# Optimization experiments

Hardware: AMD Instinct MI355X
Metric: run time of the kernel (lower is better)

The kernel has to match this reference:

```python
import jax, jax.numpy as jnp
import numpy as np

B, N, D = 256, 512, 64  # batch, positions, channels; units = spatial_units = D


def setup_inputs() -> dict:
    key = jax.random.key(0)
    ks = jax.random.split(key, 9)
    g = 1.0 / np.sqrt(D)  # glorot-ish scale for square matrices
    return {
        "x": jax.random.normal(ks[0], (B, N, D), dtype=jnp.float32),
        "Wq_t": jax.random.normal(ks[1], (D, D), dtype=jnp.float32) * g,
        "Wk_t": jax.random.normal(ks[2], (D, D), dtype=jnp.float32) * g,
        "Wv_t": jax.random.normal(ks[3], (D, D), dtype=jnp.float32) * g,
        "Wq_s": jax.random.normal(ks[4], (D, D), dtype=jnp.float32) * g,
        "Wk_s": jax.random.normal(ks[5], (D, D), dtype=jnp.float32) * g,
        "Wv_s": jax.random.normal(ks[6], (D, D), dtype=jnp.float32) * g,
        "Wd_t": jax.random.normal(ks[7], (D, D), dtype=jnp.float32) * g,
        "bd_t": jnp.zeros((D,), dtype=jnp.float32),
        "Wd_s": jax.random.normal(ks[8], (D, D), dtype=jnp.float32) * g,
        "bd_s": jnp.zeros((D,), dtype=jnp.float32),
    }


def _branch(x, Wq, Wk, Wv, Wd, bd):
    # x: [B, N, D]; one self-attention branch followed by a Dense layer.
    q = jnp.einsum("bnd,de->bne", x, Wq)
    k = jnp.einsum("bnd,de->bne", x, Wk)
    v = jnp.einsum("bnd,de->bne", x, Wv)
    scale = 1.0 / jnp.sqrt(jnp.asarray(Wk.shape[-1], dtype=x.dtype))
    scores = jnp.einsum("bne,bme->bnm", q, k) * scale  # [B, N, N]
    w = jax.nn.softmax(scores, axis=-1)
    attn = jnp.einsum("bnm,bmd->bnd", w, v)
    return jnp.einsum("bnd,de->bne", attn, Wd) + bd


def reference(x, Wq_t, Wk_t, Wv_t, Wq_s, Wk_s, Wv_s, Wd_t, bd_t, Wd_s, bd_s):
    temporal = _branch(x, Wq_t, Wk_t, Wv_t, Wd_t, bd_t)
    spatial = _branch(x, Wq_s, Wk_s, Wv_s, Wd_s, bd_s)
    gate = jax.nn.sigmoid(temporal + spatial)
    return x * gate
```

## Files before the change

### kernel.cpp

```cpp
#include <hip/hip_runtime.h>

typedef __attribute__((ext_vector_type(8))) short short8;
typedef __attribute__((ext_vector_type(4))) short short4v;
typedef __attribute__((ext_vector_type(4))) float float4v;

#define MFMA16(a, b, c) __builtin_amdgcn_mfma_f32_16x16x32_bf16((a), (b), (c), 0, 0, 0)

constexpr int kThreads = 512;
constexpr int LDS_TOTAL_BYTES = 163840;

static __device__ __forceinline__ unsigned short f2bf(float f) {
  unsigned int u = __float_as_uint(f);
  u = (u + 0x7fffu + ((u >> 16) & 1u)) >> 16;
  return (unsigned short)u;
}

static __device__ __forceinline__ int wsw_idx(int e, int d) {
  return ((((d >> 3) << 9) + (e << 3) + (d & 7)) ^ (((d >> 3) & 3) << 3));
}

__global__ __launch_bounds__(kThreads, 2) void ts_attn_fused(
    const float* __restrict__ x, const float* __restrict__ Wq_t,
    const float* __restrict__ Wk_t, const float* __restrict__ Wv_t,
    const float* __restrict__ Wq_s, const float* __restrict__ Wk_s,
    const float* __restrict__ Wv_s, const float* __restrict__ Wd_t,
    const float* __restrict__ bd_t, const float* __restrict__ Wd_s,
    const float* __restrict__ bd_s, float* __restrict__ out,
    unsigned short* __restrict__ qws) {
  extern __shared__ __align__(16) unsigned short smem[];
  unsigned short* Ksw = smem;
  unsigned short* Vsw = smem + 32768;
  unsigned short* Wst = smem + 65536;
  unsigned short* Wdsw = smem + 77824;

  const int tid = threadIdx.x;
  const int wv = tid >> 6;
  const int lane = tid & 63;
  const int ln = lane & 15;
  const int quad = lane >> 4;
  const int e8 = ln & 7;
  const int b = blockIdx.x;

  const float* xb = x + (size_t)b * (512 * 64);
  float* outb = out + (size_t)b * (512 * 64);
  unsigned short* qg = qws + (size_t)b * (512 * 64);

#pragma unroll 1
  for (int br = 0; br < 2; ++br) {
    const float* Wq = br ? Wq_s : Wq_t;
    const float* Wk = br ? Wk_s : Wk_t;
    const float* Wv = br ? Wv_s : Wv_t;
    const float* Wd = br ? Wd_s : Wd_t;

    {
      const int d = tid >> 3;
      const int e0 = (tid & 7) * 8;
      const float* srcs[3] = {Wq, Wk, Wv};
#pragma unroll
      for (int g = 0; g < 3; ++g) {
        const float4v u = *reinterpret_cast<const float4v*>(srcs[g] + d * 64 + e0);
        const float4v v = *reinterpret_cast<const float4v*>(srcs[g] + d * 64 + e0 + 4);
        unsigned short* dst = Wst + g * 4096;
#pragma unroll
        for (int i = 0; i < 4; ++i) dst[wsw_idx(e0 + i, d)] = f2bf(u[i]);
#pragma unroll
        for (int i = 0; i < 4; ++i) dst[wsw_idx(e0 + 4 + i, d)] = f2bf(v[i]);
      }
      const int cp_ = d >> 5;
      const int c = d & 31;
      const int qd_ = (c >> 2) & 3;
      const int h_ = ((c >> 4) << 2) | (c & 3);
      const int gbase = (cp_ * 4 + qd_);
      const float4v u = *reinterpret_cast<const float4v*>(Wd + d * 64 + e0);
      const float4v v = *reinterpret_cast<const float4v*>(Wd + d * 64 + e0 + 4);
#pragma unroll
      for (int i = 0; i < 4; ++i) {
        const int e = e0 + i;
        Wdsw[e * 64 + ((gbase ^ (e & 7)) << 3) + h_] = f2bf(u[i]);
      }
#pragma unroll
      for (int i = 0; i < 4; ++i) {
        const int e = e0 + 4 + i;
        Wdsw[e * 64 + ((gbase ^ (e & 7)) << 3) + h_] = f2bf(v[i]);
      }
    }
    __syncthreads();

#pragma unroll 1
    for (int mi = 0; mi < 4; ++mi) {
      const int mrow = (wv + mi * 8) * 16 + ln;
      const int kpq = mrow >> 5;
      const int w5 = mrow & 31;
      const int jj = ((w5 >> 4) << 2) | (w5 & 3);
      const int qg2 = (w5 >> 2) & 3;
      short8 xa0, xa1;
      {
        const float4v u0 = *reinterpret_cast<const float4v*>(xb + mrow * 64 + quad * 8);
        const float4v v0 = *reinterpret_cast<const float4v*>(xb + mrow * 64 + quad * 8 + 4);
        const float4v u1 = *reinterpret_cast<const float4v*>(xb + mrow * 64 + 32 + quad * 8);
        const float4v v1 = *reinterpret_cast<const float4v*>(xb + mrow * 64 + 32 + quad * 8 + 4);
#pragma unroll
        for (int i = 0; i < 4; ++i) {
          xa0[i] = (short)f2bf(u0[i]);
          xa0[4 + i] = (short)f2bf(v0[i]);
          xa1[i] = (short)f2bf(u1[i]);
          xa1[4 + i] = (short)f2bf(v1[i]);
        }
      }
#pragma unroll
      for (int g = 0; g < 3; ++g) {
        const unsigned short* Wg = Wst + g * 4096;
#pragma unroll
        for (int nt = 0; nt < 4; ++nt) {
          const short8 w0 = *reinterpret_cast<const short8*>(Wg + wsw_idx(nt * 16 + ln, quad * 8));
          const short8 w1 = *reinterpret_cast<const short8*>(Wg + wsw_idx(nt * 16 + ln, 32 + quad * 8));
          float4v acc = {0.f, 0.f, 0.f, 0.f};
          acc = MFMA16(w0, xa0, acc);
          acc = MFMA16(w1, xa1, acc);
          if (g == 0) {
            short4v pk;
#pragma unroll
            for (int r = 0; r < 4; ++r) pk[r] = (short)f2bf(acc[r]);
            *reinterpret_cast<short4v*>(
                qg + mrow * 64 + (nt >> 1) * 32 + quad * 8 + (nt & 1) * 4) = pk;
          } else if (g == 1) {
            short4v pk;
#pragma unroll
            for (int r = 0; r < 4; ++r) pk[r] = (short)f2bf(acc[r]);
            const int gswz = ((nt >> 1) * 4 + quad) ^ (mrow & 7);
            *reinterpret_cast<short4v*>(
                Ksw + mrow * 64 + (gswz << 3) + (nt & 1) * 4) = pk;
          } else {
#pragma unroll
            for (int r = 0; r < 4; ++r) {
              const int d = nt * 16 + quad * 4 + r;
              const int gv = (kpq ^ (d & 7) ^ qg2);
              Vsw[(d << 9) + (qg2 << 7) + (gv << 3) + jj] = f2bf(acc[r]);
            }
          }
        }
      }
    }
    __syncthreads();

#pragma unroll 1
    for (int qi = 0; qi < 2; ++qi) {
      const int qtA = wv + qi * 16;
      const int qtB = wv + 8 + qi * 16;
      const unsigned short* qrowA = qg + (qtA * 16 + ln) * 64;
      const unsigned short* qrowB = qg + (qtB * 16 + ln) * 64;
      const short8 qaA = *reinterpret_cast<const short8*>(qrowA + quad * 8);
      const short8 qbA = *reinterpret_cast<const short8*>(qrowA + 32 + quad * 8);
      const short8 qaB = *reinterpret_cast<const short8*>(qrowB + quad * 8);
      const short8 qbB = *reinterpret_cast<const short8*>(qrowB + 32 + quad * 8);

      const int kb0 = ln * 64 + ((quad ^ e8) << 3);
      const int kb1 = ln * 64 + (((4 + quad) ^ e8) << 3);
      const int vxor = (quad << 3) ^ (e8 << 3);

      float4v oA[4], oB[4];
#pragma unroll
      for (int i = 0; i < 4; ++i) {
        oA[i] = (float4v){0.f, 0.f, 0.f, 0.f};
        oB[i] = (float4v){0.f, 0.f, 0.f, 0.f};
      }
      float mrunA = -3.0e38f, mrunB = -3.0e38f;
      float sumA = 0.f, sumB = 0.f;

#pragma unroll 1
      for (int ch = 0; ch < 8; ++ch) {
        float4v sA[4], sB[4];
#pragma unroll
        for (int k8 = 0; k8 < 4; ++k8) {
          const int kt = ch * 4 + k8;
          const short8 k0 = *reinterpret_cast<const short8*>(Ksw + kt * 1024 + kb0);
          const short8 k1 = *reinterpret_cast<const short8*>(Ksw + kt * 1024 + kb1);
          float4v aA = {0.f, 0.f, 0.f, 0.f};
          aA = MFMA16(k0, qaA, aA);
          aA = MFMA16(k1, qbA, aA);
          sA[k8] = aA;
          float4v aB = {0.f, 0.f, 0.f, 0.f};
          aB = MFMA16(k0, qaB, aB);
          aB = MFMA16(k1, qbB, aB);
          sB[k8] = aB;
        }

        float4v m4A = sA[0], m4B = sB[0];
#pragma unroll
        for (int k8 = 1; k8 < 4; ++k8)
#pragma unroll
          for (int r = 0; r < 4; ++r) {
            m4A[r] = fmaxf(m4A[r], sA[k8][r]);
            m4B[r] = fmaxf(m4B[r], sB[k8][r]);
          }
        float cmxA = fmaxf(fmaxf(m4A[0], m4A[1]), fmaxf(m4A[2], m4A[3]));
        float cmxB = fmaxf(fmaxf(m4B[0], m4B[1]), fmaxf(m4B[2], m4B[3]));
        cmxA = fmaxf(cmxA, __shfl_xor(cmxA, 16, 64));
        cmxB = fmaxf(cmxB, __shfl_xor(cmxB, 16, 64));
        cmxA = fmaxf(cmxA, __shfl_xor(cmxA, 32, 64));
        cmxB = fmaxf(cmxB, __shfl_xor(cmxB, 32, 64));

        const float mnewA = fmaxf(mrunA, cmxA);
        const float mnewB = fmaxf(mrunB, cmxB);
        const float scaleA = __expf((mrunA - mnewA) * 0.125f);
        const float scaleB = __expf((mrunB - mnewB) * 0.125f);
        sumA *= scaleA;
        sumB *= scaleB;
#pragma unroll
        for (int i = 0; i < 4; ++i)
#pragma unroll
          for (int r = 0; r < 4; ++r) {
            oA[i][r] *= scaleA;
            oB[i][r] *= scaleB;
          }
        const float offsA = -mnewA * 0.125f;
        const float offsB = -mnewB * 0.125f;
        mrunA = mnewA;
        mrunB = mnewB;

#pragma unroll
        for (int kp = 0; kp < 2; ++kp) {
          float pA[8], pB[8];
#pragma unroll
          for (int h = 0; h < 2; ++h) {
            const int k8 = kp * 2 + h;
#pragma unroll
            for (int r = 0; r < 4; ++r) {
              pA[h * 4 + r] = __expf(fmaf(sA[k8][r], 0.125f, offsA));
              pB[h * 4 + r] = __expf(fmaf(sB[k8][r], 0.125f, offsB));
            }
          }
          sumA += ((pA[0] + pA[4]) + (pA[1] + pA[5])) + ((pA[2] + pA[6]) + (pA[3] + pA[7]));
          sumB += ((pB[0] + pB[4]) + (pB[1] + pB[5])) + ((pB[2] + pB[6]) + (pB[3] + pB[7]));
          short8 pfA, pfB;
#pragma unroll
          for (int j = 0; j < 8; ++j) {
            pfA[j] = (short)f2bf(pA[j]);
            pfB[j] = (short)f2bf(pB[j]);
          }
          const int kpg = ch * 2 + kp;
#pragma unroll
          for (int nto = 0; nto < 4; ++nto) {
            const int vb = (nto * 16 + ln) * 512 + quad * 128;
            const short8 vf = *reinterpret_cast<const short8*>(
                Vsw + vb + (((kpg << 3) ^ vxor)));
            oA[nto] = MFMA16(vf, pfA, oA[nto]);
            oB[nto] = MFMA16(vf, pfB, oB[nto]);
          }
        }
      }

      sumA += __shfl_xor(sumA, 16, 64);
      sumB += __shfl_xor(sumB, 16, 64);
      sumA += __shfl_xor(sumA, 32, 64);
      sumB += __shfl_xor(sumB, 32, 64);
      const float invA = 1.0f / sumA;
      const float invB = 1.0f / sumB;

      short8 of0A, of1A, of0B, of1B;
#pragma unroll
      for (int r = 0; r < 4; ++r) {
        of0A[r] = (short)f2bf(oA[0][r] * invA);
        of0A[4 + r] = (short)f2bf(oA[1][r] * invA);
        of1A[r] = (short)f2bf(oA[2][r] * invA);
        of1A[4 + r] = (short)f2bf(oA[3][r] * invA);
        of0B[r] = (short)f2bf(oB[0][r] * invB);
        of0B[4 + r] = (short)f2bf(oB[1][r] * invB);
        of1B[r] = (short)f2bf(oB[2][r] * invB);
        of1B[4 + r] = (short)f2bf(oB[3][r] * invB);
      }

#pragma unroll
      for (int nt = 0; nt < 4; ++nt) {
        const int ebase = (nt * 16 + ln) * 64;
        const short8 w0 = *reinterpret_cast<const short8*>(
            Wdsw + ebase + ((quad ^ e8) << 3));
        const short8 w1 = *reinterpret_cast<const short8*>(
            Wdsw + ebase + (((4 + quad) ^ e8) << 3));
        float4v accA = {0.f, 0.f, 0.f, 0.f};
        accA = MFMA16(w0, of0A, accA);
        accA = MFMA16(w1, of1A, accA);
        float4v accB = {0.f, 0.f, 0.f, 0.f};
        accB = MFMA16(w0, of0B, accB);
        accB = MFMA16(w1, of1B, accB);
        const int e0 = nt * 16 + quad * 4;
#pragma unroll
        for (int t = 0; t < 2; ++t) {
          const int row = (t == 0 ? qtA : qtB) * 16 + ln;
          const float4v acc = t == 0 ? accA : accB;
          float4v* op = reinterpret_cast<float4v*>(outb + row * 64 + e0);
          if (br == 0) {
            *op = acc;
          } else {
            const float4v bt = *reinterpret_cast<const float4v*>(bd_t + e0);
            const float4v bs = *reinterpret_cast<const float4v*>(bd_s + e0);
            const float4v parked = *op;
            const float4v xv = *reinterpret_cast<const float4v*>(xb + row * 64 + e0);
            float4v res;
#pragma unroll
            for (int r = 0; r < 4; ++r) {
              const float z = parked[r] + acc[r] + bt[r] + bs[r];
              const float gate = 1.0f / (1.0f + __expf(-z));
              res[r] = xv[r] * gate;
            }
            *op = res;
          }
        }
      }
    }
    __syncthreads();
  }
}

extern "C" void kernel_launch(void* const* d_in, const int* in_sizes, int n_in,
                              void* d_out, int out_size, void* d_ws, size_t ws_size,
                              hipStream_t stream) {
  const float* x = (const float*)d_in[0];
  const float* Wq_t = (const float*)d_in[1];
  const float* Wk_t = (const float*)d_in[2];
  const float* Wv_t = (const float*)d_in[3];
  const float* Wq_s = (const float*)d_in[4];
  const float* Wk_s = (const float*)d_in[5];
  const float* Wv_s = (const float*)d_in[6];
  const float* Wd_t = (const float*)d_in[7];
  const float* bd_t = (const float*)d_in[8];
  const float* Wd_s = (const float*)d_in[9];
  const float* bd_s = (const float*)d_in[10];
  float* out = (float*)d_out;
  unsigned short* qws = (unsigned short*)d_ws;

  hipFuncSetAttribute(reinterpret_cast<const void*>(ts_attn_fused),
                      hipFuncAttributeMaxDynamicSharedMemorySize, LDS_TOTAL_BYTES);
  ts_attn_fused<<<dim3(256), dim3(kThreads), LDS_TOTAL_BYTES, stream>>>(
      x, Wq_t, Wk_t, Wv_t, Wq_s, Wk_s, Wv_s, Wd_t, bd_t, Wd_s, bd_s, out, qws);
}
```

Measured before the change: 184.7 us.

## Split each batch across two blocks with half-size K/V LDS streaming

Launches two blocks per batch element, each owning half of the query rows, and halves the LDS footprint by holding only 256 keys of K/V at a time. The block processes the key range in two passes, recomputing K/V for the second half and restaging weights into two small slots in between. This doubles the grid and allows more resident blocks per CU, at the cost of duplicated K/V projection work and extra barriers. It also swaps the manual float-to-bf16 rounding for the native __bf16 conversion.

Measured after the change: 209.8 us. +13.6%, slower.

```diff
diff --git a/kernel.cpp b/kernel.cpp
--- a/kernel.cpp
+++ b/kernel.cpp
@@ -7,12 +7,11 @@
 #define MFMA16(a, b, c) __builtin_amdgcn_mfma_f32_16x16x32_bf16((a), (b), (c), 0, 0, 0)
 
 constexpr int kThreads = 512;
-constexpr int LDS_TOTAL_BYTES = 163840;
+constexpr int LDS_TOTAL_BYTES = 81920;
 
 static __device__ __forceinline__ unsigned short f2bf(float f) {
-  unsigned int u = __float_as_uint(f);
-  u = (u + 0x7fffu + ((u >> 16) & 1u)) >> 16;
-  return (unsigned short)u;
+  __bf16 h = (__bf16)f;
+  return __builtin_bit_cast(unsigned short, h);
 }
 
 static __device__ __forceinline__ int wsw_idx(int e, int d) {
@@ -29,9 +28,9 @@
     unsigned short* __restrict__ qws) {
   extern __shared__ __align__(16) unsigned short smem[];
   unsigned short* Ksw = smem;
-  unsigned short* Vsw = smem + 32768;
-  unsigned short* Wst = smem + 65536;
-  unsigned short* Wdsw = smem + 77824;
+  unsigned short* Vsw = smem + 16384;
+  unsigned short* slotA = smem + 32768;
+  unsigned short* slotB = smem + 36864;
 
   const int tid = threadIdx.x;
   const int wv = tid >> 6;
@@ -39,11 +38,96 @@
   const int ln = lane & 15;
   const int quad = lane >> 4;
   const int e8 = ln & 7;
-  const int b = blockIdx.x;
+  const int bp = blockIdx.x;
+  const int b = bp >> 1;
+  const int h = bp & 1;
 
   const float* xb = x + (size_t)b * (512 * 64);
   float* outb = out + (size_t)b * (512 * 64);
   unsigned short* qg = qws + (size_t)b * (512 * 64);
+
+  const int kb0 = ln * 64 + ((quad ^ e8) << 3);
+  const int kb1 = ln * 64 + (((4 + quad) ^ e8) << 3);
+  const int vxor = (quad << 3) ^ (e8 << 3);
+
+  auto stageW = [&](const float* W, unsigned short* dst) {
+    const int d = tid >> 3;
+    const int e0 = (tid & 7) * 8;
+    const float4v u = *reinterpret_cast<const float4v*>(W + d * 64 + e0);
+    const float4v v = *reinterpret_cast<const float4v*>(W + d * 64 + e0 + 4);
+#pragma unroll
+    for (int i = 0; i < 4; ++i) dst[wsw_idx(e0 + i, d)] = f2bf(u[i]);
+#pragma unroll
+    for (int i = 0; i < 4; ++i) dst[wsw_idx(e0 + 4 + i, d)] = f2bf(v[i]);
+  };
+  auto stageWd = [&](const float* W, unsigned short* dst) {
+    const int d = tid >> 3;
+    const int e0 = (tid & 7) * 8;
+    const int cp_ = d >> 5;
+    const int c = d & 31;
+    const int qd_ = (c >> 2) & 3;
+    const int h_ = ((c >> 4) << 2) | (c & 3);
+    const int gbase = cp_ * 4 + qd_;
+    const float4v u = *reinterpret_cast<const float4v*>(W + d * 64 + e0);
+    const float4v v = *reinterpret_cast<const float4v*>(W + d * 64 + e0 + 4);
+#pragma unroll
+    for (int i = 0; i < 4; ++i) {
+      const int e = e0 + i;
+      dst[e * 64 + ((gbase ^ (e & 7)) << 3) + h_] = f2bf(u[i]);
+    }
+#pragma unroll
+    for (int i = 0; i < 4; ++i) {
+      const int e = e0 + 4 + i;
+      dst[e * 64 + ((gbase ^ (e & 7)) << 3) + h_] = f2bf(v[i]);
+    }
+  };
+  auto loadX = [&](int grow, short8& xa0, short8& xa1) {
+    const float4v u0 = *reinterpret_cast<const float4v*>(xb + grow * 64 + quad * 8);
+    const float4v v0 = *reinterpret_cast<const float4v*>(xb + grow * 64 + quad * 8 + 4);
+    const float4v u1 = *reinterpret_cast<const float4v*>(xb + grow * 64 + 32 + quad * 8);
+    const float4v v1 = *reinterpret_cast<const float4v*>(xb + grow * 64 + 32 + quad * 8 + 4);
+#pragma unroll
+    for (int i = 0; i < 4; ++i) {
+      xa0[i] = (short)f2bf(u0[i]);
+      xa0[4 + i] = (short)f2bf(v0[i]);
+      xa1[i] = (short)f2bf(u1[i]);
+      xa1[4 + i] = (short)f2bf(v1[i]);
+    }
+  };
+  auto mmW = [&](const unsigned short* Wl, const short8& xa0, const short8& xa1,
+                 int nt) -> float4v {
+    const short8 w0 = *reinterpret_cast<const short8*>(Wl + wsw_idx(nt * 16 + ln, quad * 8));
+    const short8 w1 = *reinterpret_cast<const short8*>(Wl + wsw_idx(nt * 16 + ln, 32 + quad * 8));
+    float4v acc = {0.f, 0.f, 0.f, 0.f};
+    acc = MFMA16(w0, xa0, acc);
+    acc = MFMA16(w1, xa1, acc);
+    return acc;
+  };
+  auto writeQ = [&](int grow, int nt, float4v acc) {
+    short4v pk;
+#pragma unroll
+    for (int r = 0; r < 4; ++r) pk[r] = (short)f2bf(acc[r]);
+    *reinterpret_cast<short4v*>(qg + grow * 64 + (nt >> 1) * 32 + quad * 8 + (nt & 1) * 4) = pk;
+  };
+  auto writeK = [&](int lrow, int nt, float4v acc) {
+    short4v pk;
+#pragma unroll
+    for (int r = 0; r < 4; ++r) pk[r] = (short)f2bf(acc[r]);
+    const int gswz = ((nt >> 1) * 4 + quad) ^ (lrow & 7);
+    *reinterpret_cast<short4v*>(Ksw + lrow * 64 + (gswz << 3) + (nt & 1) * 4) = pk;
+  };
+  auto writeV = [&](int lrow, int nt, float4v acc) {
+    const int kpqL = lrow >> 5;
+    const int w5 = lrow & 31;
+    const int jj = ((w5 >> 4) << 2) | (w5 & 3);
+    const int qg2 = (w5 >> 2) & 3;
+#pragma unroll
+    for (int r = 0; r < 4; ++r) {
+      const int d = nt * 16 + quad * 4 + r;
+      const int gv = kpqL ^ (d & 7) ^ qg2;
+      Vsw[(d << 8) + (qg2 << 6) + (gv << 3) + jj] = f2bf(acc[r]);
+    }
+  };
 
 #pragma unroll 1
   for (int br = 0; br < 2; ++br) {
@@ -52,123 +136,62 @@
     const float* Wv = br ? Wv_s : Wv_t;
     const float* Wd = br ? Wd_s : Wd_t;
 
-    {
-      const int d = tid >> 3;
-      const int e0 = (tid & 7) * 8;
-      const float* srcs[3] = {Wq, Wk, Wv};
-#pragma unroll
-      for (int g = 0; g < 3; ++g) {
-        const float4v u = *reinterpret_cast<const float4v*>(srcs[g] + d * 64 + e0);
-        const float4v v = *reinterpret_cast<const float4v*>(srcs[g] + d * 64 + e0 + 4);
-        unsigned short* dst = Wst + g * 4096;
-#pragma unroll
-        for (int i = 0; i < 4; ++i) dst[wsw_idx(e0 + i, d)] = f2bf(u[i]);
-#pragma unroll
-        for (int i = 0; i < 4; ++i) dst[wsw_idx(e0 + 4 + i, d)] = f2bf(v[i]);
-      }
-      const int cp_ = d >> 5;
-      const int c = d & 31;
-      const int qd_ = (c >> 2) & 3;
-      const int h_ = ((c >> 4) << 2) | (c & 3);
-      const int gbase = (cp_ * 4 + qd_);
-      const float4v u = *reinterpret_cast<const float4v*>(Wd + d * 64 + e0);
-      const float4v v = *reinterpret_cast<const float4v*>(Wd + d * 64 + e0 + 4);
-#pragma unroll
-      for (int i = 0; i < 4; ++i) {
-        const int e = e0 + i;
-        Wdsw[e * 64 + ((gbase ^ (e & 7)) << 3) + h_] = f2bf(u[i]);
-      }
-#pragma unroll
-      for (int i = 0; i < 4; ++i) {
-        const int e = e0 + 4 + i;
-        Wdsw[e * 64 + ((gbase ^ (e & 7)) << 3) + h_] = f2bf(v[i]);
-      }
-    }
-    __syncthreads();
-
-#pragma unroll 1
-    for (int mi = 0; mi < 4; ++mi) {
-      const int mrow = (wv + mi * 8) * 16 + ln;
-      const int kpq = mrow >> 5;
-      const int w5 = mrow & 31;
-      const int jj = ((w5 >> 4) << 2) | (w5 & 3);
-      const int qg2 = (w5 >> 2) & 3;
+    stageW(Wq, slotA);
+    stageW(Wk, slotB);
+    __syncthreads();
+
+#pragma unroll 1
+    for (int i = 0; i < 2; ++i) {
+      const int grow = (h * 16 + wv + i * 8) * 16 + ln;
       short8 xa0, xa1;
-      {
-        const float4v u0 = *reinterpret_cast<const float4v*>(xb + mrow * 64 + quad * 8);
-        const float4v v0 = *reinterpret_cast<const float4v*>(xb + mrow * 64 + quad * 8 + 4);
-        const float4v u1 = *reinterpret_cast<const float4v*>(xb + mrow * 64 + 32 + quad * 8);
-        const float4v v1 = *reinterpret_cast<const float4v*>(xb + mrow * 64 + 32 + quad * 8 + 4);
-#pragma unroll
-        for (int i = 0; i < 4; ++i) {
-          xa0[i] = (short)f2bf(u0[i]);
-          xa0[4 + i] = (short)f2bf(v0[i]);
-          xa1[i] = (short)f2bf(u1[i]);
-          xa1[4 + i] = (short)f2bf(v1[i]);
-        }
-      }
-#pragma unroll
-      for (int g = 0; g < 3; ++g) {
-        const unsigned short* Wg = Wst + g * 4096;
-#pragma unroll
-        for (int nt = 0; nt < 4; ++nt) {
-          const short8 w0 = *reinterpret_cast<const short8*>(Wg + wsw_idx(nt * 16 + ln, quad * 8));
-          const short8 w1 = *reinterpret_cast<const short8*>(Wg + wsw_idx(nt * 16 + ln, 32 + quad * 8));
-          float4v acc = {0.f, 0.f, 0.f, 0.f};
-          acc = MFMA16(w0, xa0, acc);
-          acc = MFMA16(w1, xa1, acc);
-          if (g == 0) {
-            short4v pk;
-#pragma unroll
-            for (int r = 0; r < 4; ++r) pk[r] = (short)f2bf(acc[r]);
-            *reinterpret_cast<short4v*>(
-                qg + mrow * 64 + (nt >> 1) * 32 + quad * 8 + (nt & 1) * 4) = pk;
-          } else if (g == 1) {
-            short4v pk;
-#pragma unroll
-            for (int r = 0; r < 4; ++r) pk[r] = (short)f2bf(acc[r]);
-            const int gswz = ((nt >> 1) * 4 + quad) ^ (mrow & 7);
-            *reinterpret_cast<short4v*>(
-                Ksw + mrow * 64 + (gswz << 3) + (nt & 1) * 4) = pk;
-          } else {
-#pragma unroll
-            for (int r = 0; r < 4; ++r) {
-              const int d = nt * 16 + quad * 4 + r;
-              const int gv = (kpq ^ (d & 7) ^ qg2);
-              Vsw[(d << 9) + (qg2 << 7) + (gv << 3) + jj] = f2bf(acc[r]);
-            }
-          }
-        }
-      }
-    }
-    __syncthreads();
-
-#pragma unroll 1
-    for (int qi = 0; qi < 2; ++qi) {
-      const int qtA = wv + qi * 16;
-      const int qtB = wv + 8 + qi * 16;
-      const unsigned short* qrowA = qg + (qtA * 16 + ln) * 64;
-      const unsigned short* qrowB = qg + (qtB * 16 + ln) * 64;
-      const short8 qaA = *reinterpret_cast<const short8*>(qrowA + quad * 8);
-      const short8 qbA = *reinterpret_cast<const short8*>(qrowA + 32 + quad * 8);
-      const short8 qaB = *reinterpret_cast<const short8*>(qrowB + quad * 8);
-      const short8 qbB = *reinterpret_cast<const short8*>(qrowB + 32 + quad * 8);
-
-      const int kb0 = ln * 64 + ((quad ^ e8) << 3);
-      const int kb1 = ln * 64 + (((4 + quad) ^ e8) << 3);
-      const int vxor = (quad << 3) ^ (e8 << 3);
-
-      float4v oA[4], oB[4];
-#pragma unroll
-      for (int i = 0; i < 4; ++i) {
-        oA[i] = (float4v){0.f, 0.f, 0.f, 0.f};
-        oB[i] = (float4v){0.f, 0.f, 0.f, 0.f};
-      }
-      float mrunA = -3.0e38f, mrunB = -3.0e38f;
-      float sumA = 0.f, sumB = 0.f;
-
-#pragma unroll 1
-      for (int ch = 0; ch < 8; ++ch) {
+      loadX(grow, xa0, xa1);
+#pragma unroll
+      for (int nt = 0; nt < 4; ++nt) writeQ(grow, nt, mmW(slotA, xa0, xa1, nt));
+    }
+#pragma unroll 1
+    for (int i = 0; i < 2; ++i) {
+      const int lrow = (wv + i * 8) * 16 + ln;
+      short8 xa0, xa1;
+      loadX(lrow, xa0, xa1);
+#pragma unroll
+      for (int nt = 0; nt < 4; ++nt) writeK(lrow, nt, mmW(slotB, xa0, xa1, nt));
+    }
+    __syncthreads();
+
+    stageW(Wv, slotA);
+    __syncthreads();
+#pragma unroll 1
+    for (int i = 0; i < 2; ++i) {
+      const int lrow = (wv + i * 8) * 16 + ln;
+      short8 xa0, xa1;
+      loadX(lrow, xa0, xa1);
+#pragma unroll
+      for (int nt = 0; nt < 4; ++nt) writeV(lrow, nt, mmW(slotA, xa0, xa1, nt));
+    }
+    __syncthreads();
+
+    const int qtA = h * 16 + wv;
+    const int qtB = h * 16 + wv + 8;
+    const unsigned short* qrowA = qg + (qtA * 16 + ln) * 64;
+    const unsigned short* qrowB = qg + (qtB * 16 + ln) * 64;
+    const short8 qaA = *reinterpret_cast<const short8*>(qrowA + quad * 8);
+    const short8 qbA = *reinterpret_cast<const short8*>(qrowA + 32 + quad * 8);
+    const short8 qaB = *reinterpret_cast<const short8*>(qrowB + quad * 8);
+    const short8 qbB = *reinterpret_cast<const short8*>(qrowB + 32 + quad * 8);
+
+    float4v oA[4], oB[4];
+#pragma unroll
+    for (int i = 0; i < 4; ++i) {
+      oA[i] = (float4v){0.f, 0.f, 0.f, 0.f};
+      oB[i] = (float4v){0.f, 0.f, 0.f, 0.f};
+    }
+    float mrunA = -3.0e38f, mrunB = -3.0e38f;
+    float sumA = 0.f, sumB = 0.f;
+
+#pragma unroll 1
+    for (int p = 0; p < 2; ++p) {
+#pragma unroll 1
+      for (int ch = 0; ch < 4; ++ch) {
         float4v sA[4], sB[4];
 #pragma unroll
         for (int k8 = 0; k8 < 4; ++k8) {
@@ -222,12 +245,12 @@
         for (int kp = 0; kp < 2; ++kp) {
           float pA[8], pB[8];
 #pragma unroll
-          for (int h = 0; h < 2; ++h) {
-            const int k8 = kp * 2 + h;
+          for (int hh = 0; hh < 2; ++hh) {
+            const int k8 = kp * 2 + hh;
 #pragma unroll
             for (int r = 0; r < 4; ++r) {
-              pA[h * 4 + r] = __expf(fmaf(sA[k8][r], 0.125f, offsA));
-              pB[h * 4 + r] = __expf(fmaf(sB[k8][r], 0.125f, offsB));
+              pA[hh * 4 + r] = __expf(fmaf(sA[k8][r], 0.125f, offsA));
+              pB[hh * 4 + r] = __expf(fmaf(sB[k8][r], 0.125f, offsB));
             }
           }
           sumA += ((pA[0] + pA[4]) + (pA[1] + pA[5])) + ((pA[2] + pA[6]) + (pA[3] + pA[7]));
@@ -241,7 +264,7 @@
           const int kpg = ch * 2 + kp;
 #pragma unroll
           for (int nto = 0; nto < 4; ++nto) {
-            const int vb = (nto * 16 + ln) * 512 + quad * 128;
+            const int vb = (nto * 16 + ln) * 256 + quad * 64;
             const short8 vf = *reinterpret_cast<const short8*>(
                 Vsw + vb + (((kpg << 3) ^ vxor)));
             oA[nto] = MFMA16(vf, pfA, oA[nto]);
@@ -250,61 +273,84 @@
         }
       }
 
-      sumA += __shfl_xor(sumA, 16, 64);
-      sumB += __shfl_xor(sumB, 16, 64);
-      sumA += __shfl_xor(sumA, 32, 64);
-      sumB += __shfl_xor(sumB, 32, 64);
-      const float invA = 1.0f / sumA;
-      const float invB = 1.0f / sumB;
-
-      short8 of0A, of1A, of0B, of1B;
-#pragma unroll
-      for (int r = 0; r < 4; ++r) {
-        of0A[r] = (short)f2bf(oA[0][r] * invA);
-        of0A[4 + r] = (short)f2bf(oA[1][r] * invA);
-        of1A[r] = (short)f2bf(oA[2][r] * invA);
-        of1A[4 + r] = (short)f2bf(oA[3][r] * invA);
-        of0B[r] = (short)f2bf(oB[0][r] * invB);
-        of0B[4 + r] = (short)f2bf(oB[1][r] * invB);
-        of1B[r] = (short)f2bf(oB[2][r] * invB);
-        of1B[4 + r] = (short)f2bf(oB[3][r] * invB);
+      if (p == 0) {
+        __syncthreads();
+        stageW(Wk, slotA);
+        stageW(Wv, slotB);
+        __syncthreads();
+#pragma unroll 1
+        for (int i = 0; i < 2; ++i) {
+          const int lrow = (wv + i * 8) * 16 + ln;
+          const int grow = 256 + lrow;
+          short8 xa0, xa1;
+          loadX(grow, xa0, xa1);
+#pragma unroll
+          for (int nt = 0; nt < 4; ++nt) {
+            writeK(lrow, nt, mmW(slotA, xa0, xa1, nt));
+            writeV(lrow, nt, mmW(slotB, xa0, xa1, nt));
+          }
+        }
+        __syncthreads();
       }
-
-#pragma unroll
-      for (int nt = 0; nt < 4; ++nt) {
-        const int ebase = (nt * 16 + ln) * 64;
-        const short8 w0 = *reinterpret_cast<const short8*>(
-            Wdsw + ebase + ((quad ^ e8) << 3));
-        const short8 w1 = *reinterpret_cast<const short8*>(
-            Wdsw + ebase + (((4 + quad) ^ e8) << 3));
-        float4v accA = {0.f, 0.f, 0.f, 0.f};
-        accA = MFMA16(w0, of0A, accA);
-        accA = MFMA16(w1, of1A, accA);
-        float4v accB = {0.f, 0.f, 0.f, 0.f};
-        accB = MFMA16(w0, of0B, accB);
-        accB = MFMA16(w1, of1B, accB);
-        const int e0 = nt * 16 + quad * 4;
-#pragma unroll
-        for (int t = 0; t < 2; ++t) {
-          const int row = (t == 0 ? qtA : qtB) * 16 + ln;
-          const float4v acc = t == 0 ? accA : accB;
-          float4v* op = reinterpret_cast<float4v*>(outb + row * 64 + e0);
-          if (br == 0) {
-            *op = acc;
-          } else {
-            const float4v bt = *reinterpret_cast<const float4v*>(bd_t + e0);
-            const float4v bs = *reinterpret_cast<const float4v*>(bd_s + e0);
-            const float4v parked = *op;
-            const float4v xv = *reinterpret_cast<const float4v*>(xb + row * 64 + e0);
-            float4v res;
-#pragma unroll
-            for (int r = 0; r < 4; ++r) {
-              const float z = parked[r] + acc[r] + bt[r] + bs[r];
-              const float gate = 1.0f / (1.0f + __expf(-z));
-              res[r] = xv[r] * gate;
-            }
-            *op = res;
-          }
+    }
+
+    sumA += __shfl_xor(sumA, 16, 64);
+    sumB += __shfl_xor(sumB, 16, 64);
+    sumA += __shfl_xor(sumA, 32, 64);
+    sumB += __shfl_xor(sumB, 32, 64);
+    const float invA = 1.0f / sumA;
+    const float invB = 1.0f / sumB;
+
+    short8 of0A, of1A, of0B, of1B;
+#pragma unroll
+    for (int r = 0; r < 4; ++r) {
+      of0A[r] = (short)f2bf(oA[0][r] * invA);
+      of0A[4 + r] = (short)f2bf(oA[1][r] * invA);
+      of1A[r] = (short)f2bf(oA[2][r] * invA);
+      of1A[4 + r] = (short)f2bf(oA[3][r] * invA);
+      of0B[r] = (short)f2bf(oB[0][r] * invB);
+      of0B[4 + r] = (short)f2bf(oB[1][r] * invB);
+      of1B[r] = (short)f2bf(oB[2][r] * invB);
+      of1B[4 + r] = (short)f2bf(oB[3][r] * invB);
+    }
+
+    stageWd(Wd, slotA);
+    __syncthreads();
+
+#pragma unroll
+    for (int nt = 0; nt < 4; ++nt) {
+      const int ebase = (nt * 16 + ln) * 64;
+      const short8 w0 = *reinterpret_cast<const short8*>(
+          slotA + ebase + ((quad ^ e8) << 3));
+      const short8 w1 = *reinterpret_cast<const short8*>(
+          slotA + ebase + (((4 + quad) ^ e8) << 3));
+      float4v accA = {0.f, 0.f, 0.f, 0.f};
+      accA = MFMA16(w0, of0A, accA);
+      accA = MFMA16(w1, of1A, accA);
+      float4v accB = {0.f, 0.f, 0.f, 0.f};
+      accB = MFMA16(w0, of0B, accB);
+      accB = MFMA16(w1, of1B, accB);
+      const int e0 = nt * 16 + quad * 4;
+#pragma unroll
+      for (int t = 0; t < 2; ++t) {
+        const int row = (t == 0 ? qtA : qtB) * 16 + ln;
+        const float4v acc = t == 0 ? accA : accB;
+        float4v* op = reinterpret_cast<float4v*>(outb + row * 64 + e0);
+        if (br == 0) {
+          *op = acc;
+        } else {
+          const float4v bt = *reinterpret_cast<const float4v*>(bd_t + e0);
+          const float4v bs = *reinterpret_cast<const float4v*>(bd_s + e0);
+          const float4v parked = *op;
+          const float4v xv = *reinterpret_cast<const float4v*>(xb + row * 64 + e0);
+          float4v res;
+#pragma unroll
+          for (int r = 0; r < 4; ++r) {
+            const float z = parked[r] + acc[r] + bt[r] + bs[r];
+            const float gate = 1.0f / (1.0f + __expf(-z));
+            res[r] = xv[r] * gate;
+          }
+          *op = res;
         }
       }
     }
@@ -331,6 +377,6 @@
 
   hipFuncSetAttribute(reinterpret_cast<const void*>(ts_attn_fused),
                       hipFuncAttributeMaxDynamicSharedMemorySize, LDS_TOTAL_BYTES);
-  ts_attn_fused<<<dim3(256), dim3(kThreads), LDS_TOTAL_BYTES, stream>>>(
+  ts_attn_fused<<<dim3(512), dim3(kThreads), LDS_TOTAL_BYTES, stream>>>(
       x, Wq_t, Wk_t, Wv_t, Wq_s, Wk_s, Wv_s, Wd_t, bd_t, Wd_s, bd_s, out, qws);
 }
```
